# Kernel tuning notes

Measured on AMD Instinct MI355X. Metric: run time of the kernel, lower is better.

## Reference

```python
import jax, jax.numpy as jnp
import numpy as np

N_KERNELS = 5
MUL_FACTOR = 2.0


def setup_inputs() -> dict:
    key = jax.random.key(0)
    k1, k2 = jax.random.split(key)
    X = jax.random.normal(k1, (4096, 512), dtype=jnp.float32)
    Y = jax.random.normal(k2, (4096, 512), dtype=jnp.float32)
    return {"X": X, "Y": Y}


def _mmd(X, Y):
    # multipliers: 2.0 ** (arange(5) - 2) = [0.25, 0.5, 1, 2, 4]
    mults = MUL_FACTOR ** (jnp.arange(N_KERNELS, dtype=jnp.float32) - N_KERNELS // 2)
    Z = jnp.concatenate([X, Y], axis=0)            # [N+M, D]
    n = Z.shape[0]
    # squared euclidean pairwise distances (cdist ** 2)
    sq = jnp.sum(Z * Z, axis=-1)                    # [N+M]
    D2 = sq[:, None] + sq[None, :] - 2.0 * (Z @ Z.T)
    D2 = jnp.maximum(D2, 0.0)                       # [N+M, N+M]
    # bandwidth from detached distances: sum / (n^2 - n)
    bw = jax.lax.stop_gradient(jnp.sum(D2)) / (n * n - n)
    # multi-bandwidth RBF sum over kernels
    K = jnp.sum(jnp.exp(-D2[None, :, :] / (bw * mults)[:, None, None]), axis=0)
    Nx = X.shape[0]
    XX = jnp.mean(K[:Nx, :Nx])
    XY = jnp.mean(K[:Nx, Nx:])
    YY = jnp.mean(K[Nx:, Nx:])
    return XX - 2.0 * XY + YY


def reference(X, Y):
    return _mmd(X, Y)
```

## Files before the change

kernel.cpp:

```cpp
#include <hip/hip_runtime.h>
#include <math.h>

#define N_ROWS 8192
#define NX     4096
#define DIM    512
#define BT     128
#define NT     64
#define NTRI   2080
#define BK     32

typedef __bf16 bf16_t;
typedef bf16_t bf16x8 __attribute__((ext_vector_type(8)));
typedef float  f32x4  __attribute__((ext_vector_type(4)));

#if __has_builtin(__builtin_amdgcn_exp2f)
  #define EXP2F __builtin_amdgcn_exp2f
#else
  #define EXP2F exp2f
#endif


__device__ __forceinline__ const float* zrow(const float* X, const float* Y, int r) {
    return (r < NX) ? (X + (size_t)r * DIM) : (Y + (size_t)(r - NX) * DIM);
}

__device__ __forceinline__ void gload_lds16(const bf16_t* g, bf16_t* l) {
    __builtin_amdgcn_global_load_lds(
        (__attribute__((address_space(1))) void*)(void*)(g),
        (__attribute__((address_space(3))) void*)(void*)(l), 16, 0, 0);
}

__global__ void k_prep(const float* __restrict__ X, const float* __restrict__ Y,
                       bf16_t* __restrict__ Zh, float* __restrict__ sqrow,
                       float* __restrict__ colsum) {
    int t = threadIdx.x;
    if (blockIdx.x == 0) { colsum[t] = 0.f; colsum[t + 256] = 0.f; }
    int wv = t >> 6, lane = t & 63;
    int row = blockIdx.x * 4 + wv;
    const float4* z4 = (const float4*)zrow(X, Y, row);
    float4 a = z4[lane * 2], b = z4[lane * 2 + 1];
    bf16x8 h;
    h[0] = (bf16_t)a.x; h[1] = (bf16_t)a.y; h[2] = (bf16_t)a.z; h[3] = (bf16_t)a.w;
    h[4] = (bf16_t)b.x; h[5] = (bf16_t)b.y; h[6] = (bf16_t)b.z; h[7] = (bf16_t)b.w;
    *(bf16x8*)(Zh + (size_t)row * DIM + lane * 8) = h;
    float s = a.x*a.x + a.y*a.y + a.z*a.z + a.w*a.w
            + b.x*b.x + b.y*b.y + b.z*b.z + b.w*b.w;
    #pragma unroll
    for (int off = 32; off > 0; off >>= 1) s += __shfl_down(s, off);
    if (lane == 0) sqrow[row] = s;
}

__global__ __launch_bounds__(512) void k_colsum(const bf16_t* __restrict__ Zh,
                                                float* __restrict__ colsum) {
    __shared__ float red[8][4][8];
    int t = threadIdx.x, lane = t & 63, wv = t >> 6;
    int n16 = lane & 15, q16 = lane >> 4;
    int g = blockIdx.x & 15, slab = blockIdx.x >> 4;
    int c0 = g * 32 + q16 * 8;
    float s[8] = {0.f, 0.f, 0.f, 0.f, 0.f, 0.f, 0.f, 0.f};
    #pragma unroll
    for (int it = 0; it < 8; ++it) {
        int r = slab * 1024 + it * 128 + wv * 16 + n16;
        bf16x8 v = *(const bf16x8*)(Zh + (size_t)r * DIM + c0);
        #pragma unroll
        for (int j = 0; j < 8; ++j) s[j] += (float)v[j];
    }
    #pragma unroll
    for (int off = 8; off >= 1; off >>= 1)
        #pragma unroll
        for (int j = 0; j < 8; ++j) s[j] += __shfl_down(s[j], off);
    if (n16 == 0)
        #pragma unroll
        for (int j = 0; j < 8; ++j) red[wv][q16][j] = s[j];
    __syncthreads();
    if (t < 32) {
        int q = t >> 3, j = t & 7;
        float v = 0.f;
        #pragma unroll
        for (int w = 0; w < 8; ++w) v += red[w][q][j];
        atomicAdd(&colsum[g * 32 + q * 8 + j], v);
    }
}

__global__ void k_bw(const float* sqrow, const float* colsum, float* cvals, double* acc) {
    __shared__ double red[256];
    int t = threadIdx.x;
    double s1 = 0.0;
    for (int i = t; i < N_ROWS; i += 256) s1 += (double)sqrow[i];
    double cs = 0.0;
    for (int d = t; d < DIM; d += 256) { double v = colsum[d]; cs += v * v; }
    red[t] = s1; __syncthreads();
    for (int off = 128; off > 0; off >>= 1) { if (t < off) red[t] += red[t + off]; __syncthreads(); }
    double S1 = red[0]; __syncthreads();
    red[t] = cs; __syncthreads();
    for (int off = 128; off > 0; off >>= 1) { if (t < off) red[t] += red[t + off]; __syncthreads(); }
    if (t < 8) acc[t * 16] = 0.0;
    if (t == 0) {
        double CS = red[0];
        double n = (double)N_ROWS;
        double sumD2 = 2.0 * n * S1 - 2.0 * CS;
        double bw = sumD2 / (n * n - n);
        const double LOG2E = 1.4426950408889634;
        double mult = 0.25;
        for (int k = 0; k < 5; ++k) {
            cvals[k] = (float)(-LOG2E / (bw * mult));
            mult *= 2.0;
        }
    }
}

__global__ __launch_bounds__(256, 3) void k_pair(const bf16_t* __restrict__ Zh,
                                                 const float* __restrict__ sqrow,
                                                 const float* __restrict__ cvals,
                                                 double* __restrict__ acc) {
    int L0 = blockIdx.x;
    int L = (L0 & 7) * (NTRI / 8) + (L0 >> 3);
    int ti = (int)(NT + 0.5 - sqrt((NT + 0.5) * (NT + 0.5) - 2.0 * (double)L));
    if (ti < 0) ti = 0;
    while (ti > 0 && ti * NT - ti * (ti - 1) / 2 > L) --ti;
    while ((ti + 1) * NT - (ti + 1) * ti / 2 <= L) ++ti;
    int tj = ti + (L - (ti * NT - ti * (ti - 1) / 2));

    __shared__ bf16_t As[3][4096];
    __shared__ bf16_t Bs[3][4096];
    __shared__ float wsum[4];

    int t = threadIdx.x, lane = t & 63, wv = t >> 6;
    int wr = wv >> 1, wc = wv & 1;

    const bf16_t* gA[2]; const bf16_t* gB[2];
    {
        int c0 = t, r0 = c0 >> 2, sq0 = c0 & 3, q0 = sq0 ^ ((r0 >> 1) & 3);
        int c1 = 256 + t, r1 = c1 >> 2, sq1 = c1 & 3, q1 = sq1 ^ ((r1 >> 1) & 3);
        gA[0] = Zh + (size_t)(ti * BT + r0) * DIM + q0 * 8;
        gB[0] = Zh + (size_t)(tj * BT + r0) * DIM + q0 * 8;
        gA[1] = Zh + (size_t)(ti * BT + r1) * DIM + q1 * 8;
        gB[1] = Zh + (size_t)(tj * BT + r1) * DIM + q1 * 8;
    }
    int ldsoff0 = (wv * 64) * 8;
    int ldsoff1 = (256 + wv * 64) * 8;

    int n16 = lane & 15, q16 = lane >> 4;
    int aoff[4], boff[4];
    #pragma unroll
    for (int aa = 0; aa < 4; ++aa) {
        int r = 16 * (wr * 4 + aa) + n16;
        aoff[aa] = (r * 4 + (q16 ^ ((r >> 1) & 3))) * 8;
    }
    #pragma unroll
    for (int bb = 0; bb < 4; ++bb) {
        int r = 16 * (wc * 4 + bb) + n16;
        boff[bb] = (r * 4 + (q16 ^ ((r >> 1) & 3))) * 8;
    }

    f32x4 accf[4][4];
    #pragma unroll
    for (int a = 0; a < 4; ++a)
        #pragma unroll
        for (int b = 0; b < 4; ++b)
            accf[a][b] = (f32x4){0.f, 0.f, 0.f, 0.f};

#define STAGE(S) do {                                   \
        int _b = (S) % 3; int _kn = (S) * BK;           \
        gload_lds16(gA[0] + _kn, &As[_b][ldsoff0]);     \
        gload_lds16(gB[0] + _kn, &Bs[_b][ldsoff0]);     \
        gload_lds16(gA[1] + _kn, &As[_b][ldsoff1]);     \
        gload_lds16(gB[1] + _kn, &Bs[_b][ldsoff1]);     \
    } while (0)

#define KSTEP(S, VM, DO_STAGE) do {                                          \
        asm volatile("s_waitcnt vmcnt(" VM ")" ::: "memory");                \
        __builtin_amdgcn_s_barrier();                                        \
        __builtin_amdgcn_sched_barrier(0);                                   \
        if (DO_STAGE) STAGE((S) + 2);                                        \
        const bf16_t* Ab = &As[(S) % 3][0];                                  \
        const bf16_t* Bb = &Bs[(S) % 3][0];                                  \
        bf16x8 a[4], b[4];                                                   \
        _Pragma("unroll")                                                    \
        for (int aa = 0; aa < 4; ++aa) a[aa] = *(const bf16x8*)(Ab + aoff[aa]); \
        _Pragma("unroll")                                                    \
        for (int bb = 0; bb < 4; ++bb) b[bb] = *(const bf16x8*)(Bb + boff[bb]); \
        __builtin_amdgcn_s_setprio(1);                                       \
        _Pragma("unroll")                                                    \
        for (int aa = 0; aa < 4; ++aa)                                       \
            _Pragma("unroll")                                                \
            for (int bb = 0; bb < 4; ++bb)                                   \
                accf[aa][bb] = __builtin_amdgcn_mfma_f32_16x16x32_bf16(      \
                    a[aa], b[bb], accf[aa][bb], 0, 0, 0);                    \
        __builtin_amdgcn_s_setprio(0);                                       \
    } while (0)

    STAGE(0); STAGE(1);
    KSTEP( 0, "4", 1); KSTEP( 1, "4", 1); KSTEP( 2, "4", 1); KSTEP( 3, "4", 1);
    KSTEP( 4, "4", 1); KSTEP( 5, "4", 1); KSTEP( 6, "4", 1); KSTEP( 7, "4", 1);
    KSTEP( 8, "4", 1); KSTEP( 9, "4", 1); KSTEP(10, "4", 1); KSTEP(11, "4", 1);
    KSTEP(12, "4", 1); KSTEP(13, "4", 1);
    KSTEP(14, "4", 0);
    KSTEP(15, "0", 0);
#undef KSTEP
#undef STAGE

    float c4 = cvals[4];
    int i0 = ti * BT + wr * 64;
    int j0 = tj * BT + wc * 64;

    float sqi[4][4], sqj[4];
    #pragma unroll
    for (int aa = 0; aa < 4; ++aa)
        #pragma unroll
        for (int r = 0; r < 4; ++r)
            sqi[aa][r] = sqrow[i0 + 16 * aa + q16 * 4 + r];
    #pragma unroll
    for (int bb = 0; bb < 4; ++bb)
        sqj[bb] = sqrow[j0 + 16 * bb + n16];

    float s_local = 0.f;
    #pragma unroll
    for (int aa = 0; aa < 4; ++aa) {
        #pragma unroll
        for (int bb = 0; bb < 4; ++bb) {
            #pragma unroll
            for (int r = 0; r < 4; ++r) {
                float d2 = fmaf(-2.f, accf[aa][bb][r], sqi[aa][r] + sqj[bb]);
                d2 = fmaxf(d2, 0.f);
                float e4 = EXP2F(d2 * c4);
                float e3 = e4 * e4;
                float e2 = e3 * e3;
                float e1 = e2 * e2;
                float e0 = e1 * e1;
                s_local += e4 + e3 + e2 + e1 + e0;
            }
        }
    }
    #pragma unroll
    for (int off = 32; off > 0; off >>= 1) s_local += __shfl_down(s_local, off);
    if (lane == 0) wsum[wv] = s_local;
    __syncthreads();
    if (t == 0) {
        float bs = wsum[0] + wsum[1] + wsum[2] + wsum[3];
        double si = (ti < NT / 2) ? 1.0 : -1.0;
        double sj = (tj < NT / 2) ? 1.0 : -1.0;
        double w = si * sj * ((ti == tj) ? 1.0 : 2.0);
        atomicAdd(&acc[(L0 & 7) * 16], w * (double)bs);
    }
}

__global__ void k_final(const double* acc, float* out) {
    double s = 0.0;
    #pragma unroll
    for (int i = 0; i < 8; ++i) s += acc[i * 16];
    out[0] = (float)(s / ((double)NX * (double)NX));
}

extern "C" void kernel_launch(void* const* d_in, const int* in_sizes, int n_in,
                              void* d_out, int out_size, void* d_ws, size_t ws_size,
                              hipStream_t stream) {
    const float* X = (const float*)d_in[0];
    const float* Y = (const float*)d_in[1];
    float* out = (float*)d_out;

    float*  sqrow  = (float*)d_ws;
    float*  colsum = sqrow + 8192;
    float*  cvals  = (float*)((char*)d_ws + 34816);
    double* acc    = (double*)((char*)d_ws + 34944);
    bf16_t* Zh     = (bf16_t*)((char*)d_ws + 36864);

    k_prep  <<<2048, 256, 0, stream>>>(X, Y, Zh, sqrow, colsum);
    k_colsum<<<128, 512, 0, stream>>>(Zh, colsum);
    k_bw    <<<1, 256, 0, stream>>>(sqrow, colsum, cvals, acc);
    k_pair  <<<NTRI, 256, 0, stream>>>(Zh, sqrow, cvals, acc);
    k_final <<<1, 1, 0, stream>>>(acc, out);
}
```

Before: 135.3 us.

## Fold bandwidth and final reduction into last-block epilogues; use 8-wave pair blocks

The separate bandwidth and final-sum kernels are removed. Their work now runs in the last block to finish, found with atomic ticket counters in k_colsum and k_pair, which cuts two launches. k_pair moves from 256 to 512 threads per 128x128 tile, so each wave computes 64x32 instead of 64x64. This halves per-wave accumulators and global-to-LDS loads, with the aim of more waves in flight for latency hiding. The costs are extra atomics and fences, and less MFMA work per LDS fragment load.

```diff
diff --git a/kernel.cpp b/kernel.cpp
--- a/kernel.cpp
+++ b/kernel.cpp
@@ -32,9 +32,13 @@
 
 __global__ void k_prep(const float* __restrict__ X, const float* __restrict__ Y,
                        bf16_t* __restrict__ Zh, float* __restrict__ sqrow,
-                       float* __restrict__ colsum) {
+                       float* __restrict__ colsum, unsigned* __restrict__ tk1,
+                       double* __restrict__ S1acc) {
     int t = threadIdx.x;
-    if (blockIdx.x == 0) { colsum[t] = 0.f; colsum[t + 256] = 0.f; }
+    if (blockIdx.x == 0) {
+        colsum[t] = 0.f; colsum[t + 256] = 0.f;
+        if (t == 0) { *tk1 = 0u; *S1acc = 0.0; }
+    }
     int wv = t >> 6, lane = t & 63;
     int row = blockIdx.x * 4 + wv;
     const float4* z4 = (const float4*)zrow(X, Y, row);
@@ -51,8 +55,16 @@
 }
 
 __global__ __launch_bounds__(512) void k_colsum(const bf16_t* __restrict__ Zh,
-                                                float* __restrict__ colsum) {
+                                                const float* __restrict__ sqrow,
+                                                float* __restrict__ colsum,
+                                                float* __restrict__ cvals,
+                                                double* __restrict__ S1acc,
+                                                unsigned* __restrict__ tk1,
+                                                double* __restrict__ acc,
+                                                unsigned* __restrict__ tk2) {
     __shared__ float red[8][4][8];
+    __shared__ double dred[512];
+    __shared__ int is_last;
     int t = threadIdx.x, lane = t & 63, wv = t >> 6;
     int n16 = lane & 15, q16 = lane >> 4;
     int g = blockIdx.x & 15, slab = blockIdx.x >> 4;
@@ -80,25 +92,32 @@
         for (int w = 0; w < 8; ++w) v += red[w][q][j];
         atomicAdd(&colsum[g * 32 + q * 8 + j], v);
     }
-}
-
-__global__ void k_bw(const float* sqrow, const float* colsum, float* cvals, double* acc) {
-    __shared__ double red[256];
-    int t = threadIdx.x;
-    double s1 = 0.0;
-    for (int i = t; i < N_ROWS; i += 256) s1 += (double)sqrow[i];
-    double cs = 0.0;
-    for (int d = t; d < DIM; d += 256) { double v = colsum[d]; cs += v * v; }
-    red[t] = s1; __syncthreads();
-    for (int off = 128; off > 0; off >>= 1) { if (t < off) red[t] += red[t + off]; __syncthreads(); }
-    double S1 = red[0]; __syncthreads();
-    red[t] = cs; __syncthreads();
-    for (int off = 128; off > 0; off >>= 1) { if (t < off) red[t] += red[t + off]; __syncthreads(); }
+    if (g == 0) {
+        int i = slab * 1024 + t;
+        double d = (double)sqrow[i] + (double)sqrow[i + 512];
+        #pragma unroll
+        for (int off = 32; off > 0; off >>= 1) d += __shfl_down(d, off);
+        if (lane == 0) atomicAdd(S1acc, d);
+    }
+    __syncthreads();
+    if (t == 0) {
+        __threadfence();
+        is_last = (atomicAdd(tk1, 1u) == 127u);
+    }
+    __syncthreads();
+    if (!is_last) return;
+    float cv = atomicAdd(&colsum[t], 0.f);
+    dred[t] = (double)cv * (double)cv;
+    __syncthreads();
+    for (int off = 256; off > 0; off >>= 1) {
+        if (t < off) dred[t] += dred[t + off];
+        __syncthreads();
+    }
     if (t < 8) acc[t * 16] = 0.0;
     if (t == 0) {
-        double CS = red[0];
+        double S1 = atomicAdd(S1acc, 0.0);
         double n = (double)N_ROWS;
-        double sumD2 = 2.0 * n * S1 - 2.0 * CS;
+        double sumD2 = 2.0 * n * S1 - 2.0 * dred[0];
         double bw = sumD2 / (n * n - n);
         const double LOG2E = 1.4426950408889634;
         double mult = 0.25;
@@ -106,13 +125,16 @@
             cvals[k] = (float)(-LOG2E / (bw * mult));
             mult *= 2.0;
         }
-    }
-}
-
-__global__ __launch_bounds__(256, 3) void k_pair(const bf16_t* __restrict__ Zh,
+        *tk2 = 0u;
+    }
+}
+
+__global__ __launch_bounds__(512, 6) void k_pair(const bf16_t* __restrict__ Zh,
                                                  const float* __restrict__ sqrow,
                                                  const float* __restrict__ cvals,
-                                                 double* __restrict__ acc) {
+                                                 double* __restrict__ acc,
+                                                 unsigned* __restrict__ tk2,
+                                                 float* __restrict__ out) {
     int L0 = blockIdx.x;
     int L = (L0 & 7) * (NTRI / 8) + (L0 >> 3);
     int ti = (int)(NT + 0.5 - sqrt((NT + 0.5) * (NT + 0.5) - 2.0 * (double)L));
@@ -123,49 +145,43 @@
 
     __shared__ bf16_t As[3][4096];
     __shared__ bf16_t Bs[3][4096];
-    __shared__ float wsum[4];
+    __shared__ float wsum[8];
 
     int t = threadIdx.x, lane = t & 63, wv = t >> 6;
-    int wr = wv >> 1, wc = wv & 1;
-
-    const bf16_t* gA[2]; const bf16_t* gB[2];
+    int wr = wv >> 2, wc = wv & 3;
+
+    const bf16_t* gA; const bf16_t* gB;
     {
-        int c0 = t, r0 = c0 >> 2, sq0 = c0 & 3, q0 = sq0 ^ ((r0 >> 1) & 3);
-        int c1 = 256 + t, r1 = c1 >> 2, sq1 = c1 & 3, q1 = sq1 ^ ((r1 >> 1) & 3);
-        gA[0] = Zh + (size_t)(ti * BT + r0) * DIM + q0 * 8;
-        gB[0] = Zh + (size_t)(tj * BT + r0) * DIM + q0 * 8;
-        gA[1] = Zh + (size_t)(ti * BT + r1) * DIM + q1 * 8;
-        gB[1] = Zh + (size_t)(tj * BT + r1) * DIM + q1 * 8;
-    }
-    int ldsoff0 = (wv * 64) * 8;
-    int ldsoff1 = (256 + wv * 64) * 8;
+        int r = t >> 2, sq = t & 3, q = sq ^ ((r >> 1) & 3);
+        gA = Zh + (size_t)(ti * BT + r) * DIM + q * 8;
+        gB = Zh + (size_t)(tj * BT + r) * DIM + q * 8;
+    }
+    int ldsoff = wv * 512;
 
     int n16 = lane & 15, q16 = lane >> 4;
-    int aoff[4], boff[4];
+    int aoff[4], boff[2];
     #pragma unroll
     for (int aa = 0; aa < 4; ++aa) {
-        int r = 16 * (wr * 4 + aa) + n16;
+        int r = 64 * wr + 16 * aa + n16;
         aoff[aa] = (r * 4 + (q16 ^ ((r >> 1) & 3))) * 8;
     }
     #pragma unroll
-    for (int bb = 0; bb < 4; ++bb) {
-        int r = 16 * (wc * 4 + bb) + n16;
+    for (int bb = 0; bb < 2; ++bb) {
+        int r = 32 * wc + 16 * bb + n16;
         boff[bb] = (r * 4 + (q16 ^ ((r >> 1) & 3))) * 8;
     }
 
-    f32x4 accf[4][4];
+    f32x4 accf[4][2];
     #pragma unroll
     for (int a = 0; a < 4; ++a)
         #pragma unroll
-        for (int b = 0; b < 4; ++b)
+        for (int b = 0; b < 2; ++b)
             accf[a][b] = (f32x4){0.f, 0.f, 0.f, 0.f};
 
 #define STAGE(S) do {                                   \
         int _b = (S) % 3; int _kn = (S) * BK;           \
-        gload_lds16(gA[0] + _kn, &As[_b][ldsoff0]);     \
-        gload_lds16(gB[0] + _kn, &Bs[_b][ldsoff0]);     \
-        gload_lds16(gA[1] + _kn, &As[_b][ldsoff1]);     \
-        gload_lds16(gB[1] + _kn, &Bs[_b][ldsoff1]);     \
+        gload_lds16(gA + _kn, &As[_b][ldsoff]);         \
+        gload_lds16(gB + _kn, &Bs[_b][ldsoff]);         \
     } while (0)
 
 #define KSTEP(S, VM, DO_STAGE) do {                                          \
@@ -175,50 +191,50 @@
         if (DO_STAGE) STAGE((S) + 2);                                        \
         const bf16_t* Ab = &As[(S) % 3][0];                                  \
         const bf16_t* Bb = &Bs[(S) % 3][0];                                  \
-        bf16x8 a[4], b[4];                                                   \
+        bf16x8 a[4], b[2];                                                   \
         _Pragma("unroll")                                                    \
         for (int aa = 0; aa < 4; ++aa) a[aa] = *(const bf16x8*)(Ab + aoff[aa]); \
         _Pragma("unroll")                                                    \
-        for (int bb = 0; bb < 4; ++bb) b[bb] = *(const bf16x8*)(Bb + boff[bb]); \
+        for (int bb = 0; bb < 2; ++bb) b[bb] = *(const bf16x8*)(Bb + boff[bb]); \
         __builtin_amdgcn_s_setprio(1);                                       \
         _Pragma("unroll")                                                    \
         for (int aa = 0; aa < 4; ++aa)                                       \
             _Pragma("unroll")                                                \
-            for (int bb = 0; bb < 4; ++bb)                                   \
+            for (int bb = 0; bb < 2; ++bb)                                   \
                 accf[aa][bb] = __builtin_amdgcn_mfma_f32_16x16x32_bf16(      \
                     a[aa], b[bb], accf[aa][bb], 0, 0, 0);                    \
         __builtin_amdgcn_s_setprio(0);                                       \
     } while (0)
 
     STAGE(0); STAGE(1);
-    KSTEP( 0, "4", 1); KSTEP( 1, "4", 1); KSTEP( 2, "4", 1); KSTEP( 3, "4", 1);
-    KSTEP( 4, "4", 1); KSTEP( 5, "4", 1); KSTEP( 6, "4", 1); KSTEP( 7, "4", 1);
-    KSTEP( 8, "4", 1); KSTEP( 9, "4", 1); KSTEP(10, "4", 1); KSTEP(11, "4", 1);
-    KSTEP(12, "4", 1); KSTEP(13, "4", 1);
-    KSTEP(14, "4", 0);
+    KSTEP( 0, "2", 1); KSTEP( 1, "2", 1); KSTEP( 2, "2", 1); KSTEP( 3, "2", 1);
+    KSTEP( 4, "2", 1); KSTEP( 5, "2", 1); KSTEP( 6, "2", 1); KSTEP( 7, "2", 1);
+    KSTEP( 8, "2", 1); KSTEP( 9, "2", 1); KSTEP(10, "2", 1); KSTEP(11, "2", 1);
+    KSTEP(12, "2", 1); KSTEP(13, "2", 1);
+    KSTEP(14, "2", 0);
     KSTEP(15, "0", 0);
 #undef KSTEP
 #undef STAGE
 
     float c4 = cvals[4];
     int i0 = ti * BT + wr * 64;
-    int j0 = tj * BT + wc * 64;
-
-    float sqi[4][4], sqj[4];
+    int j0 = tj * BT + wc * 32;
+
+    float sqi[4][4], sqj[2];
     #pragma unroll
     for (int aa = 0; aa < 4; ++aa)
         #pragma unroll
         for (int r = 0; r < 4; ++r)
             sqi[aa][r] = sqrow[i0 + 16 * aa + q16 * 4 + r];
     #pragma unroll
-    for (int bb = 0; bb < 4; ++bb)
+    for (int bb = 0; bb < 2; ++bb)
         sqj[bb] = sqrow[j0 + 16 * bb + n16];
 
     float s_local = 0.f;
     #pragma unroll
     for (int aa = 0; aa < 4; ++aa) {
         #pragma unroll
-        for (int bb = 0; bb < 4; ++bb) {
+        for (int bb = 0; bb < 2; ++bb) {
             #pragma unroll
             for (int r = 0; r < 4; ++r) {
                 float d2 = fmaf(-2.f, accf[aa][bb][r], sqi[aa][r] + sqj[bb]);
@@ -237,19 +253,22 @@
     if (lane == 0) wsum[wv] = s_local;
     __syncthreads();
     if (t == 0) {
-        float bs = wsum[0] + wsum[1] + wsum[2] + wsum[3];
+        float bs = 0.f;
+        #pragma unroll
+        for (int w = 0; w < 8; ++w) bs += wsum[w];
         double si = (ti < NT / 2) ? 1.0 : -1.0;
         double sj = (tj < NT / 2) ? 1.0 : -1.0;
         double w = si * sj * ((ti == tj) ? 1.0 : 2.0);
         atomicAdd(&acc[(L0 & 7) * 16], w * (double)bs);
-    }
-}
-
-__global__ void k_final(const double* acc, float* out) {
-    double s = 0.0;
-    #pragma unroll
-    for (int i = 0; i < 8; ++i) s += acc[i * 16];
-    out[0] = (float)(s / ((double)NX * (double)NX));
+        __threadfence();
+        unsigned old = atomicAdd(tk2, 1u);
+        if (old == NTRI - 1) {
+            double ssum = 0.0;
+            #pragma unroll
+            for (int i = 0; i < 8; ++i) ssum += atomicAdd(&acc[i * 16], 0.0);
+            out[0] = (float)(ssum / ((double)NX * (double)NX));
+        }
+    }
 }
 
 extern "C" void kernel_launch(void* const* d_in, const int* in_sizes, int n_in,
@@ -259,15 +278,16 @@
     const float* Y = (const float*)d_in[1];
     float* out = (float*)d_out;
 
-    float*  sqrow  = (float*)d_ws;
-    float*  colsum = sqrow + 8192;
-    float*  cvals  = (float*)((char*)d_ws + 34816);
-    double* acc    = (double*)((char*)d_ws + 34944);
-    bf16_t* Zh     = (bf16_t*)((char*)d_ws + 36864);
-
-    k_prep  <<<2048, 256, 0, stream>>>(X, Y, Zh, sqrow, colsum);
-    k_colsum<<<128, 512, 0, stream>>>(Zh, colsum);
-    k_bw    <<<1, 256, 0, stream>>>(sqrow, colsum, cvals, acc);
-    k_pair  <<<NTRI, 256, 0, stream>>>(Zh, sqrow, cvals, acc);
-    k_final <<<1, 1, 0, stream>>>(acc, out);
-}
+    float*    sqrow  = (float*)d_ws;
+    float*    colsum = sqrow + 8192;
+    float*    cvals  = (float*)((char*)d_ws + 34816);
+    unsigned* tk1    = (unsigned*)((char*)d_ws + 34840);
+    unsigned* tk2    = (unsigned*)((char*)d_ws + 34844);
+    double*   S1acc  = (double*)((char*)d_ws + 34848);
+    double*   acc    = (double*)((char*)d_ws + 34944);
+    bf16_t*   Zh     = (bf16_t*)((char*)d_ws + 36864);
+
+    k_prep  <<<2048, 256, 0, stream>>>(X, Y, Zh, sqrow, colsum, tk1, S1acc);
+    k_colsum<<<128, 512, 0, stream>>>(Zh, sqrow, colsum, cvals, S1acc, tk1, acc, tk2);
+    k_pair  <<<NTRI, 512, 0, stream>>>(Zh, sqrow, cvals, acc, tk2, out);
+}
```

Measured after the change: 171.4 us. 26.7% more time.
